# Kernel optimization log

Measured on AMD Instinct MI355X. Metric: run time of the kernel, lower is better.

The kernel has to match this reference:

```python
import jax, jax.numpy as jnp
import numpy as np

EXP_CLAMP = 1.0e6
DENOM_EPS = 1e-10
LRELU_ALPHA = 0.01


def setup_inputs() -> dict:
    key = jax.random.key(0)
    k1, k2, k3, k4, k5, k6 = jax.random.split(key, 6)
    B, N, E, F = 4, 16384, 262144, 64
    h = jax.random.normal(k1, (B, N, F), dtype=jnp.float32)
    edge = jax.random.randint(k2, (B, E, 2), 0, N, dtype=jnp.int32)
    edge_num = jax.random.randint(k3, (B,), 1, E, dtype=jnp.int32)
    edge_weight = jax.random.uniform(k4, (B, E), dtype=jnp.float32)
    W = jax.random.normal(k5, (F, F), dtype=jnp.float32) * 0.15  # xavier-ish scale
    a = jax.random.normal(k6, (1, 2 * F), dtype=jnp.float32) * 0.12
    return {"h": h, "edge": edge, "edge_num": edge_num,
            "edge_weight": edge_weight, "W": W, "a": a}


def _seg_sum(src, idx, num_segments):
    # src: [E, ...], idx: [E] -> [num_segments, ...]
    return jax.ops.segment_sum(src, idx, num_segments=num_segments)


def reference(h, edge, edge_num, edge_weight, W, a):
    B, N, Fin = h.shape
    E = edge.shape[1]
    # linear transform: Wh = h @ W^T  -> [B, N, Fout]
    Wh = jnp.einsum('bnf,of->bno', h, W)
    ctr = edge[:, :, 0]  # [B, E]
    nbr = edge[:, :, 1]  # [B, E]
    Wh_c = jnp.take_along_axis(Wh, ctr[:, :, None], axis=1)  # [B, E, Fout]
    Wh_n = jnp.take_along_axis(Wh, nbr[:, :, None], axis=1)  # [B, E, Fout]
    a_input = jnp.concatenate([Wh_c, Wh_n], axis=-1) * edge_weight[:, :, None]
    # attention logits: leakyrelu(a_input @ a^T), squeeze to [B, E]
    att1 = jax.nn.leaky_relu(jnp.einsum('bek,k->be', a_input, a[0]), LRELU_ALPHA)
    # per-batch valid-edge mask (edges beyond edge_num zeroed, as in torch loop)
    mask = (jnp.arange(E, dtype=jnp.int32)[None, :] < edge_num[:, None])
    x_exp = jnp.clip(jnp.exp(att1), 0.0, EXP_CLAMP) * mask.astype(att1.dtype)
    # segment softmax denominator over center nodes
    denom = DENOM_EPS + jax.vmap(_seg_sum, in_axes=(0, 0, None))(x_exp, ctr, N)  # [B, N]
    att = x_exp / jnp.take_along_axis(denom, ctr, axis=1)  # [B, E]
    # weighted neighbor aggregation via scatter-add on center index
    att_Wh = Wh_n * att[:, :, None]  # masked edges already have att == 0
    h_prime = jax.vmap(_seg_sum, in_axes=(0, 0, None))(att_Wh, ctr, N)  # [B, N, Fout]
    return jax.nn.relu(h_prime)
```

## Files before the change

### kernel.cpp

```cpp
#include <hip/hip_runtime.h>

#define BB 4
#define NN 16384
#define EE 262144
#define FF 64
#define ROWS (BB * NN)
#define CAP 64

__device__ __forceinline__ unsigned short f32_to_bf16(float f) {
    unsigned int u = __float_as_uint(f);
    u += 0x7FFFu + ((u >> 16) & 1u);
    return (unsigned short)(u >> 16);
}

__global__ __launch_bounds__(256) void scsn_kernel(
    const float* __restrict__ h, const float* __restrict__ W,
    const float* __restrict__ a,
    float* __restrict__ sc, float* __restrict__ sn, int* __restrict__ cnt)
{
    __shared__ float wc[FF], wn[FF];
    const int t = threadIdx.x;

    if (blockIdx.x < 256) cnt[blockIdx.x * 256 + t] = 0;

    if (t < 128) {
        const int f = t & 63;
        const float* av = a + (t >> 6) * FF;
        float s = 0.0f;
        #pragma unroll 8
        for (int o = 0; o < FF; ++o)
            s = fmaf(av[o], W[o * FF + f], s);
        (t < 64 ? wc : wn)[f] = s;
    }
    __syncthreads();

    const int gl   = t & 15;
    const int rloc = t >> 4;
    const float4 wcv = *(const float4*)&wc[gl * 4];
    const float4 wnv = *(const float4*)&wn[gl * 4];

    for (int base = blockIdx.x * 16; base < ROWS; base += gridDim.x * 16) {
        const int row = base + rloc;
        const float4 hv = ((const float4*)h)[(size_t)row * 16 + gl];
        float s1 = hv.x * wcv.x + hv.y * wcv.y + hv.z * wcv.z + hv.w * wcv.w;
        float s2 = hv.x * wnv.x + hv.y * wnv.y + hv.z * wnv.z + hv.w * wnv.w;
        #pragma unroll
        for (int off = 8; off; off >>= 1) {
            s1 += __shfl_xor(s1, off);
            s2 += __shfl_xor(s2, off);
        }
        if (gl == 0) { sc[row] = s1; sn[row] = s2; }
    }
}

__global__ __launch_bounds__(256) void wh_bin_kernel(
    const float* __restrict__ h, const float* __restrict__ W,
    const int* __restrict__ edge, const int* __restrict__ edge_num,
    const float* __restrict__ ew,
    const float* __restrict__ sc, const float* __restrict__ sn,
    unsigned short* __restrict__ Wh, int* __restrict__ cnt,
    unsigned int* __restrict__ payload)
{
    __shared__ float Wt[FF][68];
    __shared__ float hA[64][65];

    const int t = threadIdx.x;
    for (int i = t; i < FF * FF; i += 256)
        Wt[i & 63][i >> 6] = W[i];

    const int ty = t >> 4;
    const int tx = t & 15;

    for (int tile = blockIdx.x; tile < ROWS / 64; tile += gridDim.x) {
        const int rowBase = tile * 64;
        __syncthreads();
        {
            const float4* hp = (const float4*)(h + (size_t)rowBase * FF);
            #pragma unroll
            for (int k = 0; k < 4; ++k) {
                const int i4 = t + k * 256;
                const float4 v = hp[i4];
                const int rr = i4 >> 4, cc = (i4 & 15) * 4;
                hA[rr][cc] = v.x; hA[rr][cc + 1] = v.y;
                hA[rr][cc + 2] = v.z; hA[rr][cc + 3] = v.w;
            }
        }
        __syncthreads();

        float4 acc0 = {0,0,0,0}, acc1 = {0,0,0,0}, acc2 = {0,0,0,0}, acc3 = {0,0,0,0};
        #pragma unroll
        for (int f = 0; f < FF; ++f) {
            const float4 wv = *(const float4*)&Wt[f][tx * 4];
            const float h0 = hA[ty * 4][f];
            const float h1 = hA[ty * 4 + 1][f];
            const float h2 = hA[ty * 4 + 2][f];
            const float h3 = hA[ty * 4 + 3][f];
            acc0.x = fmaf(h0, wv.x, acc0.x); acc0.y = fmaf(h0, wv.y, acc0.y);
            acc0.z = fmaf(h0, wv.z, acc0.z); acc0.w = fmaf(h0, wv.w, acc0.w);
            acc1.x = fmaf(h1, wv.x, acc1.x); acc1.y = fmaf(h1, wv.y, acc1.y);
            acc1.z = fmaf(h1, wv.z, acc1.z); acc1.w = fmaf(h1, wv.w, acc1.w);
            acc2.x = fmaf(h2, wv.x, acc2.x); acc2.y = fmaf(h2, wv.y, acc2.y);
            acc2.z = fmaf(h2, wv.z, acc2.z); acc2.w = fmaf(h2, wv.w, acc2.w);
            acc3.x = fmaf(h3, wv.x, acc3.x); acc3.y = fmaf(h3, wv.y, acc3.y);
            acc3.z = fmaf(h3, wv.z, acc3.z); acc3.w = fmaf(h3, wv.w, acc3.w);
        }
        const float4 accs[4] = {acc0, acc1, acc2, acc3};
        #pragma unroll
        for (int i = 0; i < 4; ++i) {
            const int row = rowBase + ty * 4 + i;
            ushort4 st = { f32_to_bf16(accs[i].x), f32_to_bf16(accs[i].y),
                           f32_to_bf16(accs[i].z), f32_to_bf16(accs[i].w) };
            *(ushort4*)(Wh + (size_t)row * FF + tx * 4) = st;
        }
    }

    for (int i2 = blockIdx.x * 256 + t; i2 < (BB * EE) / 2;
         i2 += gridDim.x * 256) {
        const int b  = i2 >> 17;
        const int e0 = (2 * i2) & (EE - 1);
        const int en = edge_num[b];
        if (e0 >= en) continue;
        const int4   e4 = ((const int4*)edge)[i2];
        const float2 w2 = ((const float2*)ew)[i2];
        const int row0 = b * NN + e4.x;
        const int row1 = b * NN + e4.z;
        const bool act1 = (e0 + 1 < en);

        const int pos0 = atomicAdd(&cnt[row0], 1);
        const int pos1 = act1 ? atomicAdd(&cnt[row1], 1) : CAP;

        const float* snB = sn + b * NN;
        const float sc0 = sc[row0], sn0 = snB[e4.y];
        float att0 = w2.x * (sc0 + sn0);
        att0 = att0 > 0.0f ? att0 : 0.01f * att0;
        const float xe0 = fminf(__expf(att0), 1000000.0f);
        unsigned int u0 = (__float_as_uint(xe0) + 0x2000u) & 0xFFFFC000u;
        if (pos0 < CAP)
            payload[(size_t)row0 * CAP + pos0] = u0 | (unsigned int)e4.y;

        if (act1) {
            const float sc1 = sc[row1], sn1 = snB[e4.w];
            float att1 = w2.y * (sc1 + sn1);
            att1 = att1 > 0.0f ? att1 : 0.01f * att1;
            const float xe1 = fminf(__expf(att1), 1000000.0f);
            unsigned int u1 = (__float_as_uint(xe1) + 0x2000u) & 0xFFFFC000u;
            if (pos1 < CAP)
                payload[(size_t)row1 * CAP + pos1] = u1 | (unsigned int)e4.w;
        }
    }
}

__global__ __launch_bounds__(256) void gather_kernel(
    const int* __restrict__ cnt, const unsigned int* __restrict__ payload,
    const uint2* __restrict__ Wh2,
    float* __restrict__ out)
{
    const int bi = blockIdx.x;
    const int xcd = bi & 7;
    const int batch = xcd >> 1;
    const int within = ((bi >> 3) << 1) | (xcd & 1);
    const int rg = batch * 4096 + within;

    const int lane = threadIdx.x & 63;
    const int wave = threadIdx.x >> 6;
    const int row = rg * 4 + wave;
    const int grp = lane >> 4;
    const int gl  = lane & 15;
    int deg = cnt[row];
    if (deg > CAP) deg = CAP;
    const unsigned int* pl = payload + (size_t)row * CAP;
    const uint2* WhB = Wh2 + (size_t)batch * NN * 16;

    float a0 = 0.f, a1 = 0.f, a2 = 0.f, a3 = 0.f, dsum = 0.f;
    const unsigned int p = (lane < deg) ? pl[lane] : 0u;
    for (int jj = 0; jj < deg; jj += 16) {
        const unsigned int pv0 = __shfl(p, jj + grp);
        const unsigned int pv1 = __shfl(p, jj + grp + 4);
        const unsigned int pv2 = __shfl(p, jj + grp + 8);
        const unsigned int pv3 = __shfl(p, jj + grp + 12);
        const uint2 w0 = WhB[(size_t)(pv0 & 0x3FFFu) * 16 + gl];
        const uint2 w1 = WhB[(size_t)(pv1 & 0x3FFFu) * 16 + gl];
        const uint2 w2 = WhB[(size_t)(pv2 & 0x3FFFu) * 16 + gl];
        const uint2 w3 = WhB[(size_t)(pv3 & 0x3FFFu) * 16 + gl];
        const float xe0 = __uint_as_float(pv0 & 0xFFFFC000u);
        const float xe1 = __uint_as_float(pv1 & 0xFFFFC000u);
        const float xe2 = __uint_as_float(pv2 & 0xFFFFC000u);
        const float xe3 = __uint_as_float(pv3 & 0xFFFFC000u);
        a0 = fmaf(xe0, __uint_as_float(w0.x << 16),         a0);
        a1 = fmaf(xe0, __uint_as_float(w0.x & 0xFFFF0000u), a1);
        a2 = fmaf(xe0, __uint_as_float(w0.y << 16),         a2);
        a3 = fmaf(xe0, __uint_as_float(w0.y & 0xFFFF0000u), a3);
        a0 = fmaf(xe1, __uint_as_float(w1.x << 16),         a0);
        a1 = fmaf(xe1, __uint_as_float(w1.x & 0xFFFF0000u), a1);
        a2 = fmaf(xe1, __uint_as_float(w1.y << 16),         a2);
        a3 = fmaf(xe1, __uint_as_float(w1.y & 0xFFFF0000u), a3);
        a0 = fmaf(xe2, __uint_as_float(w2.x << 16),         a0);
        a1 = fmaf(xe2, __uint_as_float(w2.x & 0xFFFF0000u), a1);
        a2 = fmaf(xe2, __uint_as_float(w2.y << 16),         a2);
        a3 = fmaf(xe2, __uint_as_float(w2.y & 0xFFFF0000u), a3);
        a0 = fmaf(xe3, __uint_as_float(w3.x << 16),         a0);
        a1 = fmaf(xe3, __uint_as_float(w3.x & 0xFFFF0000u), a1);
        a2 = fmaf(xe3, __uint_as_float(w3.y << 16),         a2);
        a3 = fmaf(xe3, __uint_as_float(w3.y & 0xFFFF0000u), a3);
        dsum += (xe0 + xe1) + (xe2 + xe3);
    }
    a0 += __shfl_xor(a0, 16); a1 += __shfl_xor(a1, 16);
    a2 += __shfl_xor(a2, 16); a3 += __shfl_xor(a3, 16);
    dsum += __shfl_xor(dsum, 16);
    a0 += __shfl_xor(a0, 32); a1 += __shfl_xor(a1, 32);
    a2 += __shfl_xor(a2, 32); a3 += __shfl_xor(a3, 32);
    dsum += __shfl_xor(dsum, 32);

    if (grp == 0) {
        const float inv = 1.0f / (1e-10f + dsum);
        float4 o;
        o.x = fmaxf(a0 * inv, 0.0f);
        o.y = fmaxf(a1 * inv, 0.0f);
        o.z = fmaxf(a2 * inv, 0.0f);
        o.w = fmaxf(a3 * inv, 0.0f);
        ((float4*)out)[(size_t)row * 16 + gl] = o;
    }
}

extern "C" void kernel_launch(void* const* d_in, const int* in_sizes, int n_in,
                              void* d_out, int out_size, void* d_ws, size_t ws_size,
                              hipStream_t stream)
{
    const float* h        = (const float*)d_in[0];
    const int*   edge     = (const int*)  d_in[1];
    const int*   edge_num = (const int*)  d_in[2];
    const float* ew       = (const float*)d_in[3];
    const float* W        = (const float*)d_in[4];
    const float* a        = (const float*)d_in[5];
    float* out = (float*)d_out;

    unsigned short* Wh = (unsigned short*)d_ws;
    float* sc        = (float*)(Wh + (size_t)BB * NN * FF);
    float* sn        = sc + ROWS;
    int*   cnt       = (int*)(sn + ROWS);
    unsigned int* payload = (unsigned int*)(cnt + ROWS);

    scsn_kernel<<<1024, 256, 0, stream>>>(h, W, a, sc, sn, cnt);

    wh_bin_kernel<<<1024, 256, 0, stream>>>(h, W, edge, edge_num, ew, sc, sn,
                                            Wh, cnt, payload);

    gather_kernel<<<ROWS / 4, 256, 0, stream>>>(cnt, payload,
                                                (const uint2*)Wh, out);
}
```

Measured before the change: 139.1 us.

## Fuse score projection into GEMM and defer attention logits to gather

Removes the separate scsn kernel by computing the per-node center and neighbor scores from the GEMM accumulators, reduced across lanes with shuffles. The binning pass now stores only the edge index and neighbor id in each payload slot. Logit, leaky-relu and exp are computed in the gather kernel, which reads edge_weight, sc and sn there. The count buffer is zeroed with a memset, and the GEMM inner loop uses float4 LDS reads of h. This saves one pass over h and removes the dependency between binning and the score computation, at the cost of extra random reads of sc, sn and edge_weight in gather.

```diff
diff --git a/kernel.cpp b/kernel.cpp
--- a/kernel.cpp
+++ b/kernel.cpp
@@ -13,52 +13,12 @@
     return (unsigned short)(u >> 16);
 }
 
-__global__ __launch_bounds__(256) void scsn_kernel(
+__global__ __launch_bounds__(256) void gemm_bin_kernel(
     const float* __restrict__ h, const float* __restrict__ W,
     const float* __restrict__ a,
-    float* __restrict__ sc, float* __restrict__ sn, int* __restrict__ cnt)
-{
-    __shared__ float wc[FF], wn[FF];
-    const int t = threadIdx.x;
-
-    if (blockIdx.x < 256) cnt[blockIdx.x * 256 + t] = 0;
-
-    if (t < 128) {
-        const int f = t & 63;
-        const float* av = a + (t >> 6) * FF;
-        float s = 0.0f;
-        #pragma unroll 8
-        for (int o = 0; o < FF; ++o)
-            s = fmaf(av[o], W[o * FF + f], s);
-        (t < 64 ? wc : wn)[f] = s;
-    }
-    __syncthreads();
-
-    const int gl   = t & 15;
-    const int rloc = t >> 4;
-    const float4 wcv = *(const float4*)&wc[gl * 4];
-    const float4 wnv = *(const float4*)&wn[gl * 4];
-
-    for (int base = blockIdx.x * 16; base < ROWS; base += gridDim.x * 16) {
-        const int row = base + rloc;
-        const float4 hv = ((const float4*)h)[(size_t)row * 16 + gl];
-        float s1 = hv.x * wcv.x + hv.y * wcv.y + hv.z * wcv.z + hv.w * wcv.w;
-        float s2 = hv.x * wnv.x + hv.y * wnv.y + hv.z * wnv.z + hv.w * wnv.w;
-        #pragma unroll
-        for (int off = 8; off; off >>= 1) {
-            s1 += __shfl_xor(s1, off);
-            s2 += __shfl_xor(s2, off);
-        }
-        if (gl == 0) { sc[row] = s1; sn[row] = s2; }
-    }
-}
-
-__global__ __launch_bounds__(256) void wh_bin_kernel(
-    const float* __restrict__ h, const float* __restrict__ W,
     const int* __restrict__ edge, const int* __restrict__ edge_num,
-    const float* __restrict__ ew,
-    const float* __restrict__ sc, const float* __restrict__ sn,
-    unsigned short* __restrict__ Wh, int* __restrict__ cnt,
+    unsigned short* __restrict__ Wh, float* __restrict__ sc,
+    float* __restrict__ sn, int* __restrict__ cnt,
     unsigned int* __restrict__ payload)
 {
     __shared__ float Wt[FF][68];
@@ -70,6 +30,8 @@
 
     const int ty = t >> 4;
     const int tx = t & 15;
+    const float4 acq = ((const float4*)a)[tx];
+    const float4 anq = ((const float4*)(a + FF))[tx];
 
     for (int tile = blockIdx.x; tile < ROWS / 64; tile += gridDim.x) {
         const int rowBase = tile * 64;
@@ -89,20 +51,47 @@
 
         float4 acc0 = {0,0,0,0}, acc1 = {0,0,0,0}, acc2 = {0,0,0,0}, acc3 = {0,0,0,0};
         #pragma unroll
-        for (int f = 0; f < FF; ++f) {
-            const float4 wv = *(const float4*)&Wt[f][tx * 4];
-            const float h0 = hA[ty * 4][f];
-            const float h1 = hA[ty * 4 + 1][f];
-            const float h2 = hA[ty * 4 + 2][f];
-            const float h3 = hA[ty * 4 + 3][f];
-            acc0.x = fmaf(h0, wv.x, acc0.x); acc0.y = fmaf(h0, wv.y, acc0.y);
-            acc0.z = fmaf(h0, wv.z, acc0.z); acc0.w = fmaf(h0, wv.w, acc0.w);
-            acc1.x = fmaf(h1, wv.x, acc1.x); acc1.y = fmaf(h1, wv.y, acc1.y);
-            acc1.z = fmaf(h1, wv.z, acc1.z); acc1.w = fmaf(h1, wv.w, acc1.w);
-            acc2.x = fmaf(h2, wv.x, acc2.x); acc2.y = fmaf(h2, wv.y, acc2.y);
-            acc2.z = fmaf(h2, wv.z, acc2.z); acc2.w = fmaf(h2, wv.w, acc2.w);
-            acc3.x = fmaf(h3, wv.x, acc3.x); acc3.y = fmaf(h3, wv.y, acc3.y);
-            acc3.z = fmaf(h3, wv.z, acc3.z); acc3.w = fmaf(h3, wv.w, acc3.w);
+        for (int fq = 0; fq < 16; ++fq) {
+            const float4 w0 = *(const float4*)&Wt[fq * 4 + 0][tx * 4];
+            const float4 w1 = *(const float4*)&Wt[fq * 4 + 1][tx * 4];
+            const float4 w2 = *(const float4*)&Wt[fq * 4 + 2][tx * 4];
+            const float4 w3 = *(const float4*)&Wt[fq * 4 + 3][tx * 4];
+            const float4 h0 = *(const float4*)&hA[ty * 4 + 0][fq * 4];
+            const float4 h1 = *(const float4*)&hA[ty * 4 + 1][fq * 4];
+            const float4 h2 = *(const float4*)&hA[ty * 4 + 2][fq * 4];
+            const float4 h3 = *(const float4*)&hA[ty * 4 + 3][fq * 4];
+            acc0.x = fmaf(h0.x, w0.x, acc0.x); acc0.y = fmaf(h0.x, w0.y, acc0.y);
+            acc0.z = fmaf(h0.x, w0.z, acc0.z); acc0.w = fmaf(h0.x, w0.w, acc0.w);
+            acc0.x = fmaf(h0.y, w1.x, acc0.x); acc0.y = fmaf(h0.y, w1.y, acc0.y);
+            acc0.z = fmaf(h0.y, w1.z, acc0.z); acc0.w = fmaf(h0.y, w1.w, acc0.w);
+            acc0.x = fmaf(h0.z, w2.x, acc0.x); acc0.y = fmaf(h0.z, w2.y, acc0.y);
+            acc0.z = fmaf(h0.z, w2.z, acc0.z); acc0.w = fmaf(h0.z, w2.w, acc0.w);
+            acc0.x = fmaf(h0.w, w3.x, acc0.x); acc0.y = fmaf(h0.w, w3.y, acc0.y);
+            acc0.z = fmaf(h0.w, w3.z, acc0.z); acc0.w = fmaf(h0.w, w3.w, acc0.w);
+            acc1.x = fmaf(h1.x, w0.x, acc1.x); acc1.y = fmaf(h1.x, w0.y, acc1.y);
+            acc1.z = fmaf(h1.x, w0.z, acc1.z); acc1.w = fmaf(h1.x, w0.w, acc1.w);
+            acc1.x = fmaf(h1.y, w1.x, acc1.x); acc1.y = fmaf(h1.y, w1.y, acc1.y);
+            acc1.z = fmaf(h1.y, w1.z, acc1.z); acc1.w = fmaf(h1.y, w1.w, acc1.w);
+            acc1.x = fmaf(h1.z, w2.x, acc1.x); acc1.y = fmaf(h1.z, w2.y, acc1.y);
+            acc1.z = fmaf(h1.z, w2.z, acc1.z); acc1.w = fmaf(h1.z, w2.w, acc1.w);
+            acc1.x = fmaf(h1.w, w3.x, acc1.x); acc1.y = fmaf(h1.w, w3.y, acc1.y);
+            acc1.z = fmaf(h1.w, w3.z, acc1.z); acc1.w = fmaf(h1.w, w3.w, acc1.w);
+            acc2.x = fmaf(h2.x, w0.x, acc2.x); acc2.y = fmaf(h2.x, w0.y, acc2.y);
+            acc2.z = fmaf(h2.x, w0.z, acc2.z); acc2.w = fmaf(h2.x, w0.w, acc2.w);
+            acc2.x = fmaf(h2.y, w1.x, acc2.x); acc2.y = fmaf(h2.y, w1.y, acc2.y);
+            acc2.z = fmaf(h2.y, w1.z, acc2.z); acc2.w = fmaf(h2.y, w1.w, acc2.w);
+            acc2.x = fmaf(h2.z, w2.x, acc2.x); acc2.y = fmaf(h2.z, w2.y, acc2.y);
+            acc2.z = fmaf(h2.z, w2.z, acc2.z); acc2.w = fmaf(h2.z, w2.w, acc2.w);
+            acc2.x = fmaf(h2.w, w3.x, acc2.x); acc2.y = fmaf(h2.w, w3.y, acc2.y);
+            acc2.z = fmaf(h2.w, w3.z, acc2.z); acc2.w = fmaf(h2.w, w3.w, acc2.w);
+            acc3.x = fmaf(h3.x, w0.x, acc3.x); acc3.y = fmaf(h3.x, w0.y, acc3.y);
+            acc3.z = fmaf(h3.x, w0.z, acc3.z); acc3.w = fmaf(h3.x, w0.w, acc3.w);
+            acc3.x = fmaf(h3.y, w1.x, acc3.x); acc3.y = fmaf(h3.y, w1.y, acc3.y);
+            acc3.z = fmaf(h3.y, w1.z, acc3.z); acc3.w = fmaf(h3.y, w1.w, acc3.w);
+            acc3.x = fmaf(h3.z, w2.x, acc3.x); acc3.y = fmaf(h3.z, w2.y, acc3.y);
+            acc3.z = fmaf(h3.z, w2.z, acc3.z); acc3.w = fmaf(h3.z, w2.w, acc3.w);
+            acc3.x = fmaf(h3.w, w3.x, acc3.x); acc3.y = fmaf(h3.w, w3.y, acc3.y);
+            acc3.z = fmaf(h3.w, w3.z, acc3.z); acc3.w = fmaf(h3.w, w3.w, acc3.w);
         }
         const float4 accs[4] = {acc0, acc1, acc2, acc3};
         #pragma unroll
@@ -111,6 +100,16 @@
             ushort4 st = { f32_to_bf16(accs[i].x), f32_to_bf16(accs[i].y),
                            f32_to_bf16(accs[i].z), f32_to_bf16(accs[i].w) };
             *(ushort4*)(Wh + (size_t)row * FF + tx * 4) = st;
+            float scv = accs[i].x * acq.x + accs[i].y * acq.y
+                      + accs[i].z * acq.z + accs[i].w * acq.w;
+            float snv = accs[i].x * anq.x + accs[i].y * anq.y
+                      + accs[i].z * anq.z + accs[i].w * anq.w;
+            #pragma unroll
+            for (int off = 8; off; off >>= 1) {
+                scv += __shfl_xor(scv, off);
+                snv += __shfl_xor(snv, off);
+            }
+            if (tx == 0) { sc[row] = scv; sn[row] = snv; }
         }
     }
 
@@ -120,32 +119,18 @@
         const int e0 = (2 * i2) & (EE - 1);
         const int en = edge_num[b];
         if (e0 >= en) continue;
-        const int4   e4 = ((const int4*)edge)[i2];
-        const float2 w2 = ((const float2*)ew)[i2];
+        const int4 e4 = ((const int4*)edge)[i2];
         const int row0 = b * NN + e4.x;
-        const int row1 = b * NN + e4.z;
-        const bool act1 = (e0 + 1 < en);
-
         const int pos0 = atomicAdd(&cnt[row0], 1);
-        const int pos1 = act1 ? atomicAdd(&cnt[row1], 1) : CAP;
-
-        const float* snB = sn + b * NN;
-        const float sc0 = sc[row0], sn0 = snB[e4.y];
-        float att0 = w2.x * (sc0 + sn0);
-        att0 = att0 > 0.0f ? att0 : 0.01f * att0;
-        const float xe0 = fminf(__expf(att0), 1000000.0f);
-        unsigned int u0 = (__float_as_uint(xe0) + 0x2000u) & 0xFFFFC000u;
         if (pos0 < CAP)
-            payload[(size_t)row0 * CAP + pos0] = u0 | (unsigned int)e4.y;
-
-        if (act1) {
-            const float sc1 = sc[row1], sn1 = snB[e4.w];
-            float att1 = w2.y * (sc1 + sn1);
-            att1 = att1 > 0.0f ? att1 : 0.01f * att1;
-            const float xe1 = fminf(__expf(att1), 1000000.0f);
-            unsigned int u1 = (__float_as_uint(xe1) + 0x2000u) & 0xFFFFC000u;
+            payload[(size_t)row0 * CAP + pos0] =
+                ((unsigned int)e0 << 14) | (unsigned int)e4.y;
+        if (e0 + 1 < en) {
+            const int row1 = b * NN + e4.z;
+            const int pos1 = atomicAdd(&cnt[row1], 1);
             if (pos1 < CAP)
-                payload[(size_t)row1 * CAP + pos1] = u1 | (unsigned int)e4.w;
+                payload[(size_t)row1 * CAP + pos1] =
+                    ((unsigned int)(e0 + 1) << 14) | (unsigned int)e4.w;
         }
     }
 }
@@ -153,6 +138,8 @@
 __global__ __launch_bounds__(256) void gather_kernel(
     const int* __restrict__ cnt, const unsigned int* __restrict__ payload,
     const uint2* __restrict__ Wh2,
+    const float* __restrict__ sc, const float* __restrict__ sn,
+    const float* __restrict__ ew,
     float* __restrict__ out)
 {
     const int bi = blockIdx.x;
@@ -171,8 +158,21 @@
     const unsigned int* pl = payload + (size_t)row * CAP;
     const uint2* WhB = Wh2 + (size_t)batch * NN * 16;
 
+    const unsigned int praw = (lane < deg) ? pl[lane] : 0u;
+    float xe;
+    {
+        const int eidx = (int)(praw >> 14);
+        const int nbr  = (int)(praw & 0x3FFFu);
+        const float we = ew[(size_t)batch * EE + eidx];
+        float att = we * (sc[row] + sn[batch * NN + nbr]);
+        att = att > 0.0f ? att : 0.01f * att;
+        xe = fminf(__expf(att), 1000000.0f);
+        if (lane >= deg) xe = 0.0f;
+    }
+    const unsigned int p = ((__float_as_uint(xe) + 0x2000u) & 0xFFFFC000u)
+                         | (praw & 0x3FFFu);
+
     float a0 = 0.f, a1 = 0.f, a2 = 0.f, a3 = 0.f, dsum = 0.f;
-    const unsigned int p = (lane < deg) ? pl[lane] : 0u;
     for (int jj = 0; jj < deg; jj += 16) {
         const unsigned int pv0 = __shfl(p, jj + grp);
         const unsigned int pv1 = __shfl(p, jj + grp + 4);
@@ -240,11 +240,11 @@
     int*   cnt       = (int*)(sn + ROWS);
     unsigned int* payload = (unsigned int*)(cnt + ROWS);
 
-    scsn_kernel<<<1024, 256, 0, stream>>>(h, W, a, sc, sn, cnt);
-
-    wh_bin_kernel<<<1024, 256, 0, stream>>>(h, W, edge, edge_num, ew, sc, sn,
-                                            Wh, cnt, payload);
-
-    gather_kernel<<<ROWS / 4, 256, 0, stream>>>(cnt, payload,
-                                                (const uint2*)Wh, out);
-}
+    hipMemsetAsync(cnt, 0, sizeof(int) * ROWS, stream);
+
+    gemm_bin_kernel<<<1024, 256, 0, stream>>>(h, W, a, edge, edge_num,
+                                              Wh, sc, sn, cnt, payload);
+
+    gather_kernel<<<ROWS / 4, 256, 0, stream>>>(cnt, payload, (const uint2*)Wh,
+                                                sc, sn, ew, out);
+}
```

Result: slower. 149.8 us (+7.7%).

## Compute Wh projection with bf16 MFMA instead of LDS-tiled FP32 FMAs

Applied to the files above, without the earlier changes.

Replaces the shared-memory tiled FP32 matmul that produces Wh with per-wave bf16 MFMA 16x16x32 instructions. W and h are loaded straight from global memory into register fragments and converted to bf16, so the LDS staging and block syncs go away. Each wave handles exactly one 16-row tile, which relies on the 1024x256 launch covering all rows. Inputs are now rounded to bf16 before multiplication, which lowers precision, and the Wh stores become scattered 2-byte writes.

```diff
diff --git a/kernel.cpp b/kernel.cpp
--- a/kernel.cpp
+++ b/kernel.cpp
@@ -6,6 +6,9 @@
 #define FF 64
 #define ROWS (BB * NN)
 #define CAP 64
+
+typedef __bf16 bf16x8 __attribute__((ext_vector_type(8)));
+typedef float  f32x4  __attribute__((ext_vector_type(4)));
 
 __device__ __forceinline__ unsigned short f32_to_bf16(float f) {
     unsigned int u = __float_as_uint(f);
@@ -53,7 +56,7 @@
     }
 }
 
-__global__ __launch_bounds__(256) void wh_bin_kernel(
+__global__ __launch_bounds__(256) void mfma_bin_kernel(
     const float* __restrict__ h, const float* __restrict__ W,
     const int* __restrict__ edge, const int* __restrict__ edge_num,
     const float* __restrict__ ew,
@@ -61,56 +64,52 @@
     unsigned short* __restrict__ Wh, int* __restrict__ cnt,
     unsigned int* __restrict__ payload)
 {
-    __shared__ float Wt[FF][68];
-    __shared__ float hA[64][65];
-
     const int t = threadIdx.x;
-    for (int i = t; i < FF * FF; i += 256)
-        Wt[i & 63][i >> 6] = W[i];
-
-    const int ty = t >> 4;
-    const int tx = t & 15;
-
-    for (int tile = blockIdx.x; tile < ROWS / 64; tile += gridDim.x) {
-        const int rowBase = tile * 64;
-        __syncthreads();
-        {
-            const float4* hp = (const float4*)(h + (size_t)rowBase * FF);
+    const int lane = t & 63;
+    const int m = lane & 15;
+    const int q = lane >> 4;
+
+    bf16x8 bfrag[4][2];
+    #pragma unroll
+    for (int nt = 0; nt < 4; ++nt) {
+        const float* wr = W + (nt * 16 + m) * FF;
+        #pragma unroll
+        for (int kh = 0; kh < 2; ++kh) {
+            const float4 v0 = *(const float4*)(wr + kh * 32 + q * 8);
+            const float4 v1 = *(const float4*)(wr + kh * 32 + q * 8 + 4);
+            bf16x8 b;
+            b[0] = (__bf16)v0.x; b[1] = (__bf16)v0.y;
+            b[2] = (__bf16)v0.z; b[3] = (__bf16)v0.w;
+            b[4] = (__bf16)v1.x; b[5] = (__bf16)v1.y;
+            b[6] = (__bf16)v1.z; b[7] = (__bf16)v1.w;
+            bfrag[nt][kh] = b;
+        }
+    }
+
+    {
+        const int waveId = (blockIdx.x * 256 + t) >> 6;
+        const int R0 = waveId * 16;
+        const float* hr = h + (size_t)(R0 + m) * FF;
+        bf16x8 af[2];
+        #pragma unroll
+        for (int kh = 0; kh < 2; ++kh) {
+            const float4 v0 = *(const float4*)(hr + kh * 32 + q * 8);
+            const float4 v1 = *(const float4*)(hr + kh * 32 + q * 8 + 4);
+            bf16x8 aa;
+            aa[0] = (__bf16)v0.x; aa[1] = (__bf16)v0.y;
+            aa[2] = (__bf16)v0.z; aa[3] = (__bf16)v0.w;
+            aa[4] = (__bf16)v1.x; aa[5] = (__bf16)v1.y;
+            aa[6] = (__bf16)v1.z; aa[7] = (__bf16)v1.w;
+            af[kh] = aa;
+        }
+        #pragma unroll
+        for (int nt = 0; nt < 4; ++nt) {
+            f32x4 acc = {0.f, 0.f, 0.f, 0.f};
+            acc = __builtin_amdgcn_mfma_f32_16x16x32_bf16(af[0], bfrag[nt][0], acc, 0, 0, 0);
+            acc = __builtin_amdgcn_mfma_f32_16x16x32_bf16(af[1], bfrag[nt][1], acc, 0, 0, 0);
             #pragma unroll
-            for (int k = 0; k < 4; ++k) {
-                const int i4 = t + k * 256;
-                const float4 v = hp[i4];
-                const int rr = i4 >> 4, cc = (i4 & 15) * 4;
-                hA[rr][cc] = v.x; hA[rr][cc + 1] = v.y;
-                hA[rr][cc + 2] = v.z; hA[rr][cc + 3] = v.w;
-            }
-        }
-        __syncthreads();
-
-        float4 acc0 = {0,0,0,0}, acc1 = {0,0,0,0}, acc2 = {0,0,0,0}, acc3 = {0,0,0,0};
-        #pragma unroll
-        for (int f = 0; f < FF; ++f) {
-            const float4 wv = *(const float4*)&Wt[f][tx * 4];
-            const float h0 = hA[ty * 4][f];
-            const float h1 = hA[ty * 4 + 1][f];
-            const float h2 = hA[ty * 4 + 2][f];
-            const float h3 = hA[ty * 4 + 3][f];
-            acc0.x = fmaf(h0, wv.x, acc0.x); acc0.y = fmaf(h0, wv.y, acc0.y);
-            acc0.z = fmaf(h0, wv.z, acc0.z); acc0.w = fmaf(h0, wv.w, acc0.w);
-            acc1.x = fmaf(h1, wv.x, acc1.x); acc1.y = fmaf(h1, wv.y, acc1.y);
-            acc1.z = fmaf(h1, wv.z, acc1.z); acc1.w = fmaf(h1, wv.w, acc1.w);
-            acc2.x = fmaf(h2, wv.x, acc2.x); acc2.y = fmaf(h2, wv.y, acc2.y);
-            acc2.z = fmaf(h2, wv.z, acc2.z); acc2.w = fmaf(h2, wv.w, acc2.w);
-            acc3.x = fmaf(h3, wv.x, acc3.x); acc3.y = fmaf(h3, wv.y, acc3.y);
-            acc3.z = fmaf(h3, wv.z, acc3.z); acc3.w = fmaf(h3, wv.w, acc3.w);
-        }
-        const float4 accs[4] = {acc0, acc1, acc2, acc3};
-        #pragma unroll
-        for (int i = 0; i < 4; ++i) {
-            const int row = rowBase + ty * 4 + i;
-            ushort4 st = { f32_to_bf16(accs[i].x), f32_to_bf16(accs[i].y),
-                           f32_to_bf16(accs[i].z), f32_to_bf16(accs[i].w) };
-            *(ushort4*)(Wh + (size_t)row * FF + tx * 4) = st;
+            for (int i = 0; i < 4; ++i)
+                Wh[(size_t)(R0 + q * 4 + i) * FF + nt * 16 + m] = f32_to_bf16(acc[i]);
         }
     }
 
@@ -130,8 +129,7 @@
         const int pos1 = act1 ? atomicAdd(&cnt[row1], 1) : CAP;
 
         const float* snB = sn + b * NN;
-        const float sc0 = sc[row0], sn0 = snB[e4.y];
-        float att0 = w2.x * (sc0 + sn0);
+        float att0 = w2.x * (sc[row0] + snB[e4.y]);
         att0 = att0 > 0.0f ? att0 : 0.01f * att0;
         const float xe0 = fminf(__expf(att0), 1000000.0f);
         unsigned int u0 = (__float_as_uint(xe0) + 0x2000u) & 0xFFFFC000u;
@@ -139,8 +137,7 @@
             payload[(size_t)row0 * CAP + pos0] = u0 | (unsigned int)e4.y;
 
         if (act1) {
-            const float sc1 = sc[row1], sn1 = snB[e4.w];
-            float att1 = w2.y * (sc1 + sn1);
+            float att1 = w2.y * (sc[row1] + snB[e4.w]);
             att1 = att1 > 0.0f ? att1 : 0.01f * att1;
             const float xe1 = fminf(__expf(att1), 1000000.0f);
             unsigned int u1 = (__float_as_uint(xe1) + 0x2000u) & 0xFFFFC000u;
@@ -242,8 +239,8 @@
 
     scsn_kernel<<<1024, 256, 0, stream>>>(h, W, a, sc, sn, cnt);
 
-    wh_bin_kernel<<<1024, 256, 0, stream>>>(h, W, edge, edge_num, ew, sc, sn,
-                                            Wh, cnt, payload);
+    mfma_bin_kernel<<<1024, 256, 0, stream>>>(h, W, edge, edge_num, ew,
+                                              sc, sn, Wh, cnt, payload);
 
     gather_kernel<<<ROWS / 4, 256, 0, stream>>>(cnt, payload,
                                                 (const uint2*)Wh, out);
```

Result: no change. 138.6 us (-0.3%).
